# Kernel tuning notes

Hardware: AMD Instinct MI355X
Metric: run time of the kernel (lower is better)

Reference implementation:

```python
import jax, jax.numpy as jnp
import numpy as np

ANCHORS = np.array([[10,13],[16,30],[33,23],[30,61],[62,45],[59,119],[116,90],[156,198],[373,326]], dtype=np.float32)
STRIDES = [32, 16, 8]
GROUPS = [2, 1, 0]  # anchor_masks [[6,7,8],[3,4,5],[0,1,2]] -> group index = mask[0]//3
N_CLASSES = 80
IGNORE_THRESH = 0.7


def _safe_log(x):
    # replicates torch BCELoss log clamp at -100, NaN-safe under grad
    ok = x > 0
    return jnp.where(ok, jnp.log(jnp.where(ok, x, 1.0)), -100.0)


def _bce_sum(o, t, w=None):
    l = -(t * _safe_log(o) + (1.0 - t) * _safe_log(1.0 - o))
    if w is not None:
        l = l * w
    return jnp.sum(l)


def _layer_loss(raw, labels, stride, group):
    dtype = raw.dtype
    B, C, H, W = raw.shape
    nch = 5 + N_CLASSES
    A = 3
    fsize = H
    T = labels.shape[1]
    all_grid = jnp.asarray(ANCHORS).astype(dtype) / stride          # [9,2] anchors in grid units
    manch = all_grid[3 * group:3 * group + 3]                        # [3,2]

    # ---- make_pred ----
    o = raw.reshape(B, A, nch, H, W).transpose(0, 1, 3, 4, 2)        # [B,A,H,W,nch]
    out = jnp.concatenate([jax.nn.sigmoid(o[..., :2]), o[..., 2:4], jax.nn.sigmoid(o[..., 4:])], axis=-1)
    xs = jnp.arange(W, dtype=dtype)
    ys = jnp.arange(H, dtype=dtype)
    px = out[..., 0] + xs                                            # broadcast over W
    py = out[..., 1] + ys[:, None]
    pw = jnp.exp(o[..., 2]) * manch[:, 0][:, None, None]
    ph = jnp.exp(o[..., 3]) * manch[:, 1][:, None, None]
    pred = jnp.stack([px, py, pw, ph], axis=-1)                      # [B,A,H,W,4] (cx,cy,w,h)

    # ---- truths ----
    tx = labels[..., 1] * fsize
    ty = labels[..., 2] * fsize
    tw = labels[..., 3] * fsize
    th = labels[..., 4] * fsize
    valid = jnp.sum(labels, axis=-1) > 0                             # [B,T]
    gi = tx.astype(jnp.int32)                                        # truncation (coords >= 0)
    gj = ty.astype(jnp.int32)

    # ---- anchor matching: aligned-wh IoU vs all 9 anchors ----
    mw = jnp.minimum(tw[..., None], all_grid[:, 0])                  # [B,T,9]
    mh = jnp.minimum(th[..., None], all_grid[:, 1])
    en = ((mw > 0) & (mh > 0)).astype(dtype)
    inter = mw * mh * en
    a_iou = inter / (tw[..., None] * th[..., None] + all_grid[:, 0] * all_grid[:, 1] - inter)
    best_all = jnp.argmax(a_iou, axis=-1)                            # [B,T]
    best_n = best_all % 3
    sel = valid & ((best_all // 3) == group)

    # ---- ignore mask from pred IoU (xywh) ----
    predf = pred.reshape(B, -1, 4)                                   # [B,N,4], N=A*H*W
    truth = jnp.stack([tx, ty, tw, th], axis=-1)                     # [B,T,4]
    a_tl = predf[:, :, None, :2] - predf[:, :, None, 2:] * 0.5
    a_br = predf[:, :, None, :2] + predf[:, :, None, 2:] * 0.5
    b_tl = truth[:, None, :, :2] - truth[:, None, :, 2:] * 0.5
    b_br = truth[:, None, :, :2] + truth[:, None, :, 2:] * 0.5
    tl = jnp.maximum(a_tl, b_tl)
    br = jnp.minimum(a_br, b_br)
    enp = jnp.all(tl < br, axis=-1).astype(dtype)
    ai = jnp.prod(br - tl, axis=-1) * enp                            # [B,N,T]
    area_a = predf[:, :, 2] * predf[:, :, 3]
    area_b = truth[:, :, 2] * truth[:, :, 3]
    piou = ai / (area_a[:, :, None] + area_b[:, None, :] - ai)
    piou = jnp.where(valid[:, None, :], piou, 0.0)
    obj_mask = (~(jnp.max(piou, axis=-1) > IGNORE_THRESH)).astype(dtype).reshape(B, A, H, W)

    # ---- scatter matched targets (unmatched routed OOB and dropped) ----
    bidx = jnp.broadcast_to(jnp.arange(B)[:, None], (B, T))
    a_s = jnp.where(sel, best_n, A)                                  # A is out of bounds -> dropped
    obj_mask = obj_mask.at[bidx, a_s, gj, gi].set(1.0, mode='drop')
    tm1 = jnp.zeros((B, A, H, W), dtype).at[bidx, a_s, gj, gi].set(1.0, mode='drop')
    scale = jnp.sqrt(2.0 - tw * th / float(fsize * fsize))
    ts1 = jnp.zeros((B, A, H, W), dtype).at[bidx, a_s, gj, gi].set(scale, mode='drop')

    aw = manch[best_n, 0]
    ah = manch[best_n, 1]
    onehot = jax.nn.one_hot(labels[..., 0].astype(jnp.int32), N_CLASSES, dtype=dtype)
    v = jnp.concatenate([
        (tx - gi.astype(dtype))[..., None],
        (ty - gj.astype(dtype))[..., None],
        jnp.log(tw / aw + 1e-16)[..., None],
        jnp.log(th / ah + 1e-16)[..., None],
        jnp.ones_like(tx)[..., None],
        onehot,
    ], axis=-1)                                                      # [B,T,nch]
    target = jnp.zeros((B, A, H, W, nch), dtype).at[bidx, a_s, gj, gi].set(v, mode='drop')

    # ---- losses ----
    tm = tm1[..., None]
    ts = ts1[..., None]
    o_xy = out[..., :2] * tm
    t_xy = target[..., :2] * tm
    o_wh = out[..., 2:4] * tm * ts
    t_wh = target[..., 2:4] * tm * ts
    o_ob = out[..., 4] * obj_mask
    t_ob = target[..., 4] * obj_mask
    o_cl = out[..., 5:] * tm
    t_cl = target[..., 5:] * tm

    loss_xy = _bce_sum(o_xy, t_xy, ts * ts)
    loss_wh = 0.5 * jnp.sum((o_wh - t_wh) ** 2)
    loss_obj = _bce_sum(o_ob, t_ob)
    loss_cls = _bce_sum(o_cl, t_cl)
    return loss_xy + loss_wh + loss_obj + loss_cls


def setup_inputs() -> dict:
    key = jax.random.key(0)
    ks = jax.random.split(key, 7)
    B, T = 16, 50
    out0 = jax.random.normal(ks[0], (B, 255, 19, 19), jnp.float32)
    out1 = jax.random.normal(ks[1], (B, 255, 38, 38), jnp.float32)
    out2 = jax.random.normal(ks[2], (B, 255, 76, 76), jnp.float32)
    cls = jax.random.randint(ks[3], (B, T, 1), 0, N_CLASSES).astype(jnp.float32)
    xy = jax.random.uniform(ks[4], (B, T, 2), jnp.float32, 0.1, 0.9)
    wh = jax.random.uniform(ks[5], (B, T, 2), jnp.float32, 0.05, 0.3)
    labels = jnp.concatenate([cls, xy, wh], axis=-1)
    nvalid = jax.random.randint(ks[6], (B, 1), 1, T + 1)
    vmask = (jnp.arange(T)[None, :] < nvalid).astype(jnp.float32)
    targets = labels * vmask[..., None]                              # padded rows are all-zero
    return {"out0": out0, "out1": out1, "out2": out2, "targets": targets}


def reference(out0, out1, out2, targets):
    outs = [out0, out1, out2]
    total = jnp.zeros((), outs[0].dtype)
    for layer in range(3):
        total = total + _layer_loss(outs[layer], targets, STRIDES[layer], GROUPS[layer])
    return total
```

## Files before the change

kernel.cpp:

```cpp
#include <hip/hip_runtime.h>
#include <math.h>

#define T_TGT 50
#define NCLS 80
#define NBATCH 16

#define NB_L0 5
#define NB_L1 17
#define NB_L2 68
#define NB_MAIN ((NB_L0 + NB_L1 + NB_L2) * NBATCH)
#define N_CLS_UNITS (T_TGT * NBATCH * 3)
#define NB_CLS ((N_CLS_UNITS + 3) / 4)
#define NB_TOTAL (NB_MAIN + NB_CLS)


__constant__ float c_anchors[18] = {10,13,16,30,33,23,30,61,62,45,
                                    59,119,116,90,156,198,373,326};

__device__ __forceinline__ float softplusf(float x){
    return fmaxf(x, 0.f) + log1pf(expf(-fabsf(x)));
}
__device__ __forceinline__ float bcef(float x, float t){
    return t * softplusf(-x) + (1.f - t) * softplusf(x);
}

struct TgtMeta {
    float4 box;
    float2 misc;
    float fx, fy;
    float lw, lh;
    float w2;
};

template<int H, int STRIDE, int GROUP>
__device__ float main_cells(const float* __restrict__ raw,
                            const float* __restrict__ targets,
                            int b, int cb, int tid, TgtMeta* s_t)
{
    constexpr int HH = H * H;
    constexpr int CELLS = 3 * HH;

    const int c = cb * 256 + tid;
    const bool cell_ok = (c < CELLS);
    int a = 0, j = 0, i = 0;
    float x0 = 0.f, x1 = 0.f, x2 = 0.f, x3 = 0.f, x4 = 0.f;
    if (cell_ok) {
        a = c / HH;
        const int rem = c - a * HH;
        j = rem / H;
        i = rem - j * H;
        const float* base = raw + ((size_t)b * 255 + a * 85) * HH + rem;
        x0 = base[0];
        x1 = base[HH];
        x2 = base[2 * HH];
        x3 = base[3 * HH];
        x4 = base[4 * HH];
    }

    if (tid < T_TGT) {
        const float* lab = targets + ((size_t)b * T_TGT + tid) * 5;
        float cf = lab[0], x = lab[1], y = lab[2], w = lab[3], h = lab[4];
        bool valid = (cf + x + y + w + h) > 0.f;
        const float fs = (float)H;
        float tx = x * fs, ty = y * fs, tw = w * fs, th = h * fs;
        int gi = (int)tx, gj = (int)ty;
        float tarea = tw * th;
        float best = -1.f; int bestn = 0;
        #pragma unroll
        for (int n = 0; n < 9; n++) {
            float aw = c_anchors[2*n]   * (1.f / STRIDE);
            float ah = c_anchors[2*n+1] * (1.f / STRIDE);
            float mw = fminf(tw, aw), mh = fminf(th, ah);
            float inter = (mw > 0.f && mh > 0.f) ? mw * mh : 0.f;
            float iou = inter / (tarea + aw * ah - inter);
            if (iou > best) { best = iou; bestn = n; }
        }
        bool sel = valid && ((bestn / 3) == GROUP);
        int bn = bestn % 3;
        int key = sel ? ((bn << 20) | (gj << 10) | gi) : -1;
        s_t[tid].box  = make_float4(tx - tw*0.5f, ty - th*0.5f,
                                    tx + tw*0.5f, ty + th*0.5f);
        s_t[tid].misc = make_float2(0.7f * tarea, __int_as_float(key));
        s_t[tid].w2 = 2.f - tarea / (fs * fs);
        float awm = c_anchors[2*(3*GROUP + bn)]   * (1.f / STRIDE);
        float ahm = c_anchors[2*(3*GROUP + bn)+1] * (1.f / STRIDE);
        s_t[tid].lw = logf(tw / awm + 1e-16f);
        s_t[tid].lh = logf(th / ahm + 1e-16f);
        s_t[tid].fx = tx - (float)gi;
        s_t[tid].fy = ty - (float)gj;
    }
    __syncthreads();

    float local = 0.f;
    if (cell_ok) {
        float s0 = 1.f / (1.f + expf(-x0));
        float s1 = 1.f / (1.f + expf(-x1));
        float manw = c_anchors[2*(3*GROUP + a)]   * (1.f / STRIDE);
        float manh = c_anchors[2*(3*GROUP + a)+1] * (1.f / STRIDE);
        float px = s0 + (float)i, py = s1 + (float)j;
        float pw = expf(x2) * manw, ph = expf(x3) * manh;
        float atlx = px - pw * 0.5f, atly = py - ph * 0.5f;
        float abrx = px + pw * 0.5f, abry = py + ph * 0.5f;
        float carea_a = 0.7f * (pw * ph);
        const int mykey = (a << 20) | (j << 10) | i;

        int winner = -1;
        bool ign = false;
        #pragma unroll 10
        for (int t = 0; t < T_TGT; t++) {
            float4 bx = s_t[t].box;
            float2 mi = s_t[t].misc;
            float tlx = fmaxf(atlx, bx.x);
            float tly = fmaxf(atly, bx.y);
            float brx = fminf(abrx, bx.z);
            float bry = fminf(abry, bx.w);
            float dx = brx - tlx, dy = bry - tly;
            float mn = fminf(dx, dy);
            ign = ign || ((mn > 0.f) &
                          (fmaf(1.7f, dx * dy, -carea_a) > mi.x));
            if (__float_as_int(mi.y) == mykey) winner = t;
        }

        if (winner >= 0) {
            local += softplusf(-x4);
            float w2 = s_t[winner].w2;
            local += w2 * (bcef(x0, s_t[winner].fx) + bcef(x1, s_t[winner].fy));
            float dw = x2 - s_t[winner].lw;
            float dh = x3 - s_t[winner].lh;
            local += 0.5f * w2 * (dw * dw + dh * dh);
        } else if (!ign) {
            local += softplusf(x4);
        }
    }
    return local;
}

__device__ float class_unit(const float* __restrict__ r0,
                            const float* __restrict__ r1,
                            const float* __restrict__ r2,
                            const float* __restrict__ targets,
                            int u, int lane)
{
    const int L   = u / (T_TGT * NBATCH);
    const int rem = u - L * (T_TGT * NBATCH);
    const int b   = rem / T_TGT;
    const int t0  = rem - b * T_TGT;

    const int Hs[3] = {19, 38, 76};
    const float inv_s[3] = {1.f/32.f, 1.f/16.f, 1.f/8.f};
    const int Gs[3] = {2, 1, 0};
    const float* raw = (L == 0) ? r0 : (L == 1) ? r1 : r2;
    const int H = Hs[L];
    const int HH = H * H;
    const float is = inv_s[L];
    const int group = Gs[L];

    int selkey = 0x40000000 | lane;
    int clsid = 0;
    if (lane < T_TGT) {
        const float* lab = targets + ((size_t)b * T_TGT + lane) * 5;
        float cf = lab[0], x = lab[1], y = lab[2], w = lab[3], h = lab[4];
        bool valid = (cf + x + y + w + h) > 0.f;
        float fs = (float)H;
        float tx = x * fs, ty = y * fs, tw = w * fs, th = h * fs;
        float tarea = tw * th;
        float best = -1.f; int bestn = 0;
        #pragma unroll
        for (int n = 0; n < 9; n++) {
            float aw = c_anchors[2*n] * is, ah = c_anchors[2*n+1] * is;
            float mw = fminf(tw, aw), mh = fminf(th, ah);
            float inter = (mw > 0.f && mh > 0.f) ? mw * mh : 0.f;
            float iou = inter / (tarea + aw * ah - inter);
            if (iou > best) { best = iou; bestn = n; }
        }
        if (valid && (bestn / 3) == group) {
            int bn = bestn % 3, gi = (int)tx, gj = (int)ty;
            selkey = (bn << 20) | (gj << 10) | gi;
        }
        clsid = (int)cf;
    }

    const int k0 = __shfl(selkey, t0);
    bool active = !(k0 & 0x40000000);
    unsigned long long dup = __ballot(selkey == k0);
    active = active && !(dup >> (t0 + 1));

    float local = 0.f;
    if (active) {
        const int cls0 = __shfl(clsid, t0);
        const int gi = k0 & 1023, gj = (k0 >> 10) & 1023, bn = k0 >> 20;
        const float* base = raw + ((size_t)b * 255 + bn * 85) * HH + gj * H + gi;
        float xc = base[(size_t)(5 + lane) * HH];
        local = softplusf(xc) - ((lane == cls0) ? xc : 0.f);
        if (lane < 16) {
            float xh = base[(size_t)(69 + lane) * HH];
            local += softplusf(xh) - ((lane + 64 == cls0) ? xh : 0.f);
        }
    }
    return local;
}

__global__ __launch_bounds__(256)
void yolo_fused(const float* __restrict__ r0,
                const float* __restrict__ r1,
                const float* __restrict__ r2,
                const float* __restrict__ targets,
                float* __restrict__ partial)
{
    __shared__ TgtMeta s_t[T_TGT];
    __shared__ float s_wsum[4];

    const int blk = blockIdx.x;
    const int tid = threadIdx.x;
    float local = 0.f;

    if (blk < NB_L0 * NBATCH) {
        int b = blk / NB_L0, cb = blk - b * NB_L0;
        local = main_cells<19, 32, 2>(r0, targets, b, cb, tid, s_t);
    } else if (blk < (NB_L0 + NB_L1) * NBATCH) {
        int q = blk - NB_L0 * NBATCH;
        int b = q / NB_L1, cb = q - b * NB_L1;
        local = main_cells<38, 16, 1>(r1, targets, b, cb, tid, s_t);
    } else if (blk < NB_MAIN) {
        int q = blk - (NB_L0 + NB_L1) * NBATCH;
        int b = q / NB_L2, cb = q - b * NB_L2;
        local = main_cells<76, 8, 0>(r2, targets, b, cb, tid, s_t);
    } else {
        int u = (blk - NB_MAIN) * 4 + (tid >> 6);
        if (u < N_CLS_UNITS)
            local = class_unit(r0, r1, r2, targets, u, tid & 63);
    }

    for (int off = 32; off > 0; off >>= 1)
        local += __shfl_down(local, off, 64);
    const int lane = tid & 63, wv = tid >> 6;
    if (lane == 0) s_wsum[wv] = local;
    __syncthreads();
    if (tid == 0)
        partial[blk] = s_wsum[0] + s_wsum[1] + s_wsum[2] + s_wsum[3];
}

__global__ __launch_bounds__(256)
void yolo_reduce(const float4* __restrict__ partial4, float* __restrict__ out)
{
    const int tid = threadIdx.x;
    constexpr int NV = NB_TOTAL / 4;
    float4 v = partial4[tid];
    float s = v.x + v.y + v.z + v.w;
    if (tid + 256 < NV) {
        float4 u = partial4[tid + 256];
        s += u.x + u.y + u.z + u.w;
    }
    for (int off = 32; off > 0; off >>= 1)
        s += __shfl_down(s, off, 64);
    __shared__ float w[4];
    if ((tid & 63) == 0) w[tid >> 6] = s;
    __syncthreads();
    if (tid == 0) out[0] = w[0] + w[1] + w[2] + w[3];
}

extern "C" void kernel_launch(void* const* d_in, const int* in_sizes, int n_in,
                              void* d_out, int out_size, void* d_ws, size_t ws_size,
                              hipStream_t stream)
{
    const float* out0 = (const float*)d_in[0];
    const float* out1 = (const float*)d_in[1];
    const float* out2 = (const float*)d_in[2];
    const float* tgt  = (const float*)d_in[3];
    float* out = (float*)d_out;
    float* partial = (float*)d_ws;

    yolo_fused<<<NB_TOTAL, 256, 0, stream>>>(out0, out1, out2, tgt, partial);
    yolo_reduce<<<1, 256, 0, stream>>>((const float4*)partial, out);
}
```

Measured before the change: 151.6 us.

## Scatter target winners via atomics and compact valid targets for early-exit ignore loop

Instead of each cell scanning all 50 targets to find a matching key, targets scatter their index into a per-block shared winner array with atomicMax (last target wins, matching the old loop). Valid targets are compacted with a ballot/popcount prefix so the IoU ignore loop only runs over valid boxes. The loop is unrolled by four and exits early once every lane in the wave is already ignored. The shared layout also changes from array-of-structs to struct-of-arrays, and an extra barrier is added for the scatter.

New measurement: 148.0 us. 1.02x faster.

```diff
diff --git a/kernel.cpp b/kernel.cpp
--- a/kernel.cpp
+++ b/kernel.cpp
@@ -24,18 +24,22 @@
     return t * softplusf(-x) + (1.f - t) * softplusf(x);
 }
 
-struct TgtMeta {
-    float4 box;
-    float2 misc;
-    float fx, fy;
-    float lw, lh;
-    float w2;
+struct SmemMain {
+    float4 box[T_TGT];
+    float  thr[T_TGT];
+    float  fx[T_TGT];
+    float  fy[T_TGT];
+    float  lw[T_TGT];
+    float  lh[T_TGT];
+    float  w2[T_TGT];
+    int    win[256];
+    int    nval;
 };
 
 template<int H, int STRIDE, int GROUP>
 __device__ float main_cells(const float* __restrict__ raw,
                             const float* __restrict__ targets,
-                            int b, int cb, int tid, TgtMeta* s_t)
+                            int b, int cb, int tid, SmemMain* sm)
 {
     constexpr int HH = H * H;
     constexpr int CELLS = 3 * HH;
@@ -57,80 +61,108 @@
         x4 = base[4 * HH];
     }
 
-    if (tid < T_TGT) {
-        const float* lab = targets + ((size_t)b * T_TGT + tid) * 5;
-        float cf = lab[0], x = lab[1], y = lab[2], w = lab[3], h = lab[4];
-        bool valid = (cf + x + y + w + h) > 0.f;
-        const float fs = (float)H;
-        float tx = x * fs, ty = y * fs, tw = w * fs, th = h * fs;
-        int gi = (int)tx, gj = (int)ty;
-        float tarea = tw * th;
-        float best = -1.f; int bestn = 0;
-        #pragma unroll
-        for (int n = 0; n < 9; n++) {
-            float aw = c_anchors[2*n]   * (1.f / STRIDE);
-            float ah = c_anchors[2*n+1] * (1.f / STRIDE);
-            float mw = fminf(tw, aw), mh = fminf(th, ah);
-            float inter = (mw > 0.f && mh > 0.f) ? mw * mh : 0.f;
-            float iou = inter / (tarea + aw * ah - inter);
-            if (iou > best) { best = iou; bestn = n; }
-        }
-        bool sel = valid && ((bestn / 3) == GROUP);
-        int bn = bestn % 3;
-        int key = sel ? ((bn << 20) | (gj << 10) | gi) : -1;
-        s_t[tid].box  = make_float4(tx - tw*0.5f, ty - th*0.5f,
-                                    tx + tw*0.5f, ty + th*0.5f);
-        s_t[tid].misc = make_float2(0.7f * tarea, __int_as_float(key));
-        s_t[tid].w2 = 2.f - tarea / (fs * fs);
-        float awm = c_anchors[2*(3*GROUP + bn)]   * (1.f / STRIDE);
-        float ahm = c_anchors[2*(3*GROUP + bn)+1] * (1.f / STRIDE);
-        s_t[tid].lw = logf(tw / awm + 1e-16f);
-        s_t[tid].lh = logf(th / ahm + 1e-16f);
-        s_t[tid].fx = tx - (float)gi;
-        s_t[tid].fy = ty - (float)gj;
+    sm->win[tid] = -1;
+
+    bool scat = false; int rel = 0;
+    if (tid < 64) {
+        bool valid = false;
+        float tx = 0.f, ty = 0.f, tw = 0.f, th = 0.f, tarea = 0.f;
+        int bestn = 0;
+        if (tid < T_TGT) {
+            const float* lab = targets + ((size_t)b * T_TGT + tid) * 5;
+            float cf = lab[0], x = lab[1], y = lab[2], w = lab[3], h = lab[4];
+            valid = (cf + x + y + w + h) > 0.f;
+            const float fs = (float)H;
+            tx = x * fs; ty = y * fs; tw = w * fs; th = h * fs;
+            tarea = tw * th;
+            float best = -1.f;
+            #pragma unroll
+            for (int n = 0; n < 9; n++) {
+                float aw = c_anchors[2*n]   * (1.f / STRIDE);
+                float ah = c_anchors[2*n+1] * (1.f / STRIDE);
+                float mw = fminf(tw, aw), mh = fminf(th, ah);
+                float inter = (mw > 0.f && mh > 0.f) ? mw * mh : 0.f;
+                float iou = inter / (tarea + aw * ah - inter);
+                if (iou > best) { best = iou; bestn = n; }
+            }
+        }
+        const unsigned long long vm = __ballot(valid);
+        if (valid) {
+            const int idx = __popcll(vm & ((1ull << tid) - 1ull));
+            sm->box[idx] = make_float4(tx - tw*0.5f, ty - th*0.5f,
+                                       tx + tw*0.5f, ty + th*0.5f);
+            sm->thr[idx] = 0.7f * tarea;
+            const int gi = (int)tx, gj = (int)ty;
+            sm->fx[tid] = tx - (float)gi;
+            sm->fy[tid] = ty - (float)gj;
+            const int bn = bestn % 3;
+            const float awm = c_anchors[2*(3*GROUP + bn)]   * (1.f / STRIDE);
+            const float ahm = c_anchors[2*(3*GROUP + bn)+1] * (1.f / STRIDE);
+            sm->lw[tid] = logf(tw / awm + 1e-16f);
+            sm->lh[tid] = logf(th / ahm + 1e-16f);
+            sm->w2[tid] = 2.f - tarea / ((float)H * (float)H);
+            if (((bestn / 3) == GROUP) &&
+                ((unsigned)gi < (unsigned)H) && ((unsigned)gj < (unsigned)H)) {
+                const int ct = bn * HH + gj * H + gi;
+                rel = ct - cb * 256;
+                scat = (rel >= 0) && (rel < 256);
+            }
+        }
+        if (tid == 0) sm->nval = __popcll(vm);
     }
     __syncthreads();
+    if (scat) atomicMax(&sm->win[rel], tid);
+    __syncthreads();
 
     float local = 0.f;
+    const int winner = sm->win[tid];
+
+    float atlx = 0.f, atly = 0.f, abrx = 0.f, abry = 0.f, carea_a = 0.f;
     if (cell_ok) {
-        float s0 = 1.f / (1.f + expf(-x0));
-        float s1 = 1.f / (1.f + expf(-x1));
-        float manw = c_anchors[2*(3*GROUP + a)]   * (1.f / STRIDE);
-        float manh = c_anchors[2*(3*GROUP + a)+1] * (1.f / STRIDE);
-        float px = s0 + (float)i, py = s1 + (float)j;
-        float pw = expf(x2) * manw, ph = expf(x3) * manh;
-        float atlx = px - pw * 0.5f, atly = py - ph * 0.5f;
-        float abrx = px + pw * 0.5f, abry = py + ph * 0.5f;
-        float carea_a = 0.7f * (pw * ph);
-        const int mykey = (a << 20) | (j << 10) | i;
-
-        int winner = -1;
-        bool ign = false;
-        #pragma unroll 10
-        for (int t = 0; t < T_TGT; t++) {
-            float4 bx = s_t[t].box;
-            float2 mi = s_t[t].misc;
-            float tlx = fmaxf(atlx, bx.x);
-            float tly = fmaxf(atly, bx.y);
-            float brx = fminf(abrx, bx.z);
-            float bry = fminf(abry, bx.w);
-            float dx = brx - tlx, dy = bry - tly;
-            float mn = fminf(dx, dy);
-            ign = ign || ((mn > 0.f) &
-                          (fmaf(1.7f, dx * dy, -carea_a) > mi.x));
-            if (__float_as_int(mi.y) == mykey) winner = t;
-        }
-
-        if (winner >= 0) {
-            local += softplusf(-x4);
-            float w2 = s_t[winner].w2;
-            local += w2 * (bcef(x0, s_t[winner].fx) + bcef(x1, s_t[winner].fy));
-            float dw = x2 - s_t[winner].lw;
-            float dh = x3 - s_t[winner].lh;
-            local += 0.5f * w2 * (dw * dw + dh * dh);
-        } else if (!ign) {
-            local += softplusf(x4);
-        }
+        const float s0 = 1.f / (1.f + expf(-x0));
+        const float s1 = 1.f / (1.f + expf(-x1));
+        const float manw = c_anchors[2*(3*GROUP + a)]   * (1.f / STRIDE);
+        const float manh = c_anchors[2*(3*GROUP + a)+1] * (1.f / STRIDE);
+        const float px = s0 + (float)i, py = s1 + (float)j;
+        const float pw = expf(x2) * manw, ph = expf(x3) * manh;
+        atlx = px - pw * 0.5f; atly = py - ph * 0.5f;
+        abrx = px + pw * 0.5f; abry = py + ph * 0.5f;
+        carea_a = 0.7f * (pw * ph);
+    }
+
+    bool ign = (!cell_ok) || (winner >= 0);
+    const int nval = sm->nval;
+
+    #define IGN_BODY(tt) {                                          \
+        const float4 bx = sm->box[tt];                              \
+        const float thr = sm->thr[tt];                              \
+        const float tlx = fmaxf(atlx, bx.x);                        \
+        const float tly = fmaxf(atly, bx.y);                        \
+        const float brx = fminf(abrx, bx.z);                        \
+        const float bry = fminf(abry, bx.w);                        \
+        const float dx = brx - tlx, dy = bry - tly;                 \
+        ign = ign || ((fminf(dx, dy) > 0.f) &&                      \
+                      (fmaf(1.7f, dx * dy, -carea_a) > thr)); }
+
+    int t = 0;
+    while (t + 4 <= nval) {
+        if (__all(ign)) break;
+        IGN_BODY(t) IGN_BODY(t+1) IGN_BODY(t+2) IGN_BODY(t+3)
+        t += 4;
+    }
+    if (!__all(ign))
+        for (; t < nval; ++t) IGN_BODY(t)
+    #undef IGN_BODY
+
+    if (winner >= 0) {
+        local += softplusf(-x4);
+        const float w2v = sm->w2[winner];
+        local += w2v * (bcef(x0, sm->fx[winner]) + bcef(x1, sm->fy[winner]));
+        const float dw = x2 - sm->lw[winner];
+        const float dh = x3 - sm->lh[winner];
+        local += 0.5f * w2v * (dw * dw + dh * dh);
+    } else if (!ign) {
+        local += softplusf(x4);
     }
     return local;
 }
@@ -207,7 +239,7 @@
                 const float* __restrict__ targets,
                 float* __restrict__ partial)
 {
-    __shared__ TgtMeta s_t[T_TGT];
+    __shared__ SmemMain sm;
     __shared__ float s_wsum[4];
 
     const int blk = blockIdx.x;
@@ -216,15 +248,15 @@
 
     if (blk < NB_L0 * NBATCH) {
         int b = blk / NB_L0, cb = blk - b * NB_L0;
-        local = main_cells<19, 32, 2>(r0, targets, b, cb, tid, s_t);
+        local = main_cells<19, 32, 2>(r0, targets, b, cb, tid, &sm);
     } else if (blk < (NB_L0 + NB_L1) * NBATCH) {
         int q = blk - NB_L0 * NBATCH;
         int b = q / NB_L1, cb = q - b * NB_L1;
-        local = main_cells<38, 16, 1>(r1, targets, b, cb, tid, s_t);
+        local = main_cells<38, 16, 1>(r1, targets, b, cb, tid, &sm);
     } else if (blk < NB_MAIN) {
         int q = blk - (NB_L0 + NB_L1) * NBATCH;
         int b = q / NB_L2, cb = q - b * NB_L2;
-        local = main_cells<76, 8, 0>(r2, targets, b, cb, tid, s_t);
+        local = main_cells<76, 8, 0>(r2, targets, b, cb, tid, &sm);
     } else {
         int u = (blk - NB_MAIN) * 4 + (tid >> 6);
         if (u < N_CLS_UNITS)
```
